# Optimization experiments

Measured on AMD Instinct MI355X. Metric: run time of the kernel, lower is better.

Reference implementation:

```python
import jax, jax.numpy as jnp
import numpy as np

H = 16          # num_heads
LN_EPS = 1e-5


def _layernorm(x, g, b):
    mu = jnp.mean(x, axis=-1, keepdims=True)
    var = jnp.mean(jnp.square(x - mu), axis=-1, keepdims=True)
    return (x - mu) * jax.lax.rsqrt(var + LN_EPS) * g + b


def setup_inputs() -> dict:
    key = jax.random.key(0)
    ks = jax.random.split(key, 4)
    B, T, D = 32, 1024, 1024
    s = 1.0 / np.sqrt(D)
    return {
        "x": jax.random.normal(ks[0], (B, T, D), dtype=jnp.float32),
        "ln_g": jnp.ones((D,), jnp.float32),
        "ln_b": jnp.zeros((D,), jnp.float32),
        "Wq": jax.random.normal(ks[1], (D, D), dtype=jnp.float32) * s,
        "bq": jnp.zeros((D,), jnp.float32),
        "Wk": jax.random.normal(ks[2], (D, D), dtype=jnp.float32) * s,
        "bk": jnp.zeros((D,), jnp.float32),
        "Wv": jax.random.normal(ks[3], (D, D), dtype=jnp.float32) * s,
        "bv": jnp.zeros((D,), jnp.float32),
    }


def reference(x, ln_g, ln_b, Wq, bq, Wk, bk, Wv, bv):
    B, T, D = x.shape
    d = D // H
    xn = _layernorm(x, ln_g, ln_b)                       # [B,T,D]
    # torch Linear: y = x @ W.T + b, W is [out, in]
    q = jnp.einsum('btd,ed->bte', xn, Wq) + bq
    k = jnp.einsum('btd,ed->bte', xn, Wk) + bk
    v = (jnp.einsum('btd,ed->bte', xn, Wv) + bv).reshape(B, T, H, d)
    q = jax.nn.softmax(q.reshape(B, T, H, d), axis=-1)   # softmax over head dim
    k = jax.nn.softmax(k.reshape(B, T, H, d), axis=1)    # softmax over sequence
    # linear attention: context [B,H,d,d], then project queries through it
    attn = jnp.einsum('bnhd,bnhl->bhdl', k, v)
    y = jnp.einsum('bnhd,bhdl->bnhl', q, attn).reshape(B, T, D)
    return x + y
```

## Files before the change

kernel.cpp:

```cpp
#include <hip/hip_runtime.h>
#include <stdint.h>

typedef __attribute__((ext_vector_type(4))) float  f32x4;
typedef __attribute__((ext_vector_type(8))) short  short8;
typedef __attribute__((ext_vector_type(2))) unsigned int uint2v;

#define DEV __device__ __forceinline__

DEV float b2f(unsigned short u) { return __uint_as_float(((unsigned)u) << 16); }
DEV unsigned short f2b(float f) {
  unsigned u = __float_as_uint(f);
  return (unsigned short)((u + 0x7fffu + ((u >> 16) & 1u)) >> 16);
}

#define AS1C(p) ((const __attribute__((address_space(1))) void*)(uintptr_t)(p))
#define AS3(p)  ((__attribute__((address_space(3))) void*)(unsigned)(uintptr_t)(p))
DEV void gload16(const void* g, void* l) {
  __builtin_amdgcn_global_load_lds(AS1C(g), AS3(l), 16, 0, 0);
}

static constexpr int B_ = 32, T_ = 1024, D_ = 1024;
static constexpr int M_ = B_ * T_;
static constexpr int N3 = 3 * D_;

__global__ __launch_bounds__(256) void cvt_weights(
    const float* __restrict__ Wq, const float* __restrict__ Wk, const float* __restrict__ Wv,
    const float* __restrict__ bq, const float* __restrict__ bk, const float* __restrict__ bv,
    unsigned short* __restrict__ Wcat, float* __restrict__ bias,
    float* __restrict__ ksum)
{
  int idx = blockIdx.x * 256 + threadIdx.x;
  int which = idx >> 18;
  int rem   = idx & 262143;
  const float* src = which == 0 ? Wq : (which == 1 ? Wk : Wv);
  f32x4 v = reinterpret_cast<const f32x4*>(src)[rem];
  uint2v p;
  p[0] = (unsigned)f2b(v[0]) | ((unsigned)f2b(v[1]) << 16);
  p[1] = (unsigned)f2b(v[2]) | ((unsigned)f2b(v[3]) << 16);
  reinterpret_cast<uint2v*>(Wcat)[idx] = p;
  if (idx < 3072) {
    const float* bsrc = idx < 1024 ? bq : (idx < 2048 ? bk : bv);
    bias[idx] = bsrc[idx & 1023];
  }
  if (idx < 32768) ksum[idx] = 0.f;
}

__global__ __launch_bounds__(256) void ln_kernel(
    const float* __restrict__ x, const float* __restrict__ g, const float* __restrict__ b,
    unsigned short* __restrict__ xn)
{
  int row = blockIdx.x;
  int tid = threadIdx.x;
  const f32x4 v = reinterpret_cast<const f32x4*>(x + (size_t)row * D_)[tid];
  float s  = v[0] + v[1] + v[2] + v[3];
  float s2 = v[0]*v[0] + v[1]*v[1] + v[2]*v[2] + v[3]*v[3];
  #pragma unroll
  for (int o = 32; o > 0; o >>= 1) { s += __shfl_down(s, o); s2 += __shfl_down(s2, o); }
  __shared__ float rs_[4], rs2_[4];
  int lane = tid & 63, wave = tid >> 6;
  if (lane == 0) { rs_[wave] = s; rs2_[wave] = s2; }
  __syncthreads();
  float S  = rs_[0] + rs_[1] + rs_[2] + rs_[3];
  float S2 = rs2_[0] + rs2_[1] + rs2_[2] + rs2_[3];
  float mu = S * (1.f / D_);
  float var = S2 * (1.f / D_) - mu * mu;
  float rstd = rsqrtf(var + 1e-5f);
  const f32x4 gg = reinterpret_cast<const f32x4*>(g)[tid];
  const f32x4 bb = reinterpret_cast<const f32x4*>(b)[tid];
  float y0 = (v[0]-mu)*rstd*gg[0] + bb[0];
  float y1 = (v[1]-mu)*rstd*gg[1] + bb[1];
  float y2 = (v[2]-mu)*rstd*gg[2] + bb[2];
  float y3 = (v[3]-mu)*rstd*gg[3] + bb[3];
  uint2v p;
  p[0] = (unsigned)f2b(y0) | ((unsigned)f2b(y1) << 16);
  p[1] = (unsigned)f2b(y2) | ((unsigned)f2b(y3) << 16);
  reinterpret_cast<uint2v*>(xn + (size_t)row * D_)[tid] = p;
}

__global__ __launch_bounds__(512, 2) void gemm_qkv(
    const unsigned short* __restrict__ A,
    const unsigned short* __restrict__ Bm,
    const float* __restrict__ bias,
    unsigned short* __restrict__ C,
    float* __restrict__ ksum)
{
  __shared__ alignas(16) short lds[4 * 16384];
  const int tid = threadIdx.x;
  constexpr int nbn = N3 / 256;
  constexpr int nwg = (M_ / 256) * nbn;
  int wg = blockIdx.x;
  int swzb = (wg & 7) * (nwg >> 3) + (wg >> 3);
  int bm = swzb / nbn, bn = swzb % nbn;
  int arow = bm * 256, bcol = bn * 256;
  int lane = tid & 63, wave = tid >> 6;
  int wr = wave >> 2, wc = wave & 3;
  int g = lane >> 4, r = lane & 15;

  const unsigned short* Ab = A  + (size_t)arow * 1024;
  const unsigned short* Bb = Bm + (size_t)bcol * 1024;

  int rho = (wave << 4) | (lane >> 2);
  int pg  = (lane & 3) ^ ((rho >> 1) & 3);
  size_t gR0 = (size_t)rho * 1024 + pg * 8;
  size_t gR1 = (size_t)(rho + 128) * 1024 + pg * 8;
  int lofs = wave * 512;

  #define STAGE_A(t) { short* bb0 = lds + (((t) & 3) << 14); int k2 = (t) << 5; \
    gload16(Ab + k2 + gR0, (void*)(bb0 + lofs)); \
    gload16(Ab + k2 + gR1, (void*)(bb0 + 4096 + lofs)); }
  #define STAGE_B(t) { short* bb0 = lds + (((t) & 3) << 14); int k2 = (t) << 5; \
    gload16(Bb + k2 + gR0, (void*)(bb0 + 8192 + lofs)); \
    gload16(Bb + k2 + gR1, (void*)(bb0 + 12288 + lofs)); }

  f32x4 acc[8][4] = {};
  STAGE_A(0); STAGE_B(0);
  STAGE_A(1); STAGE_B(1);
  STAGE_A(2); STAGE_B(2);
  asm volatile("s_waitcnt vmcnt(8)" ::: "memory");
  __builtin_amdgcn_s_barrier();

  for (int t = 0; t < 32; ++t) {
    const short* bufA = lds + ((t & 3) << 14);
    const short* bufB = bufA + 8192;
    short8 a0[4], b0[4];
    #pragma unroll
    for (int mi = 0; mi < 4; ++mi) {
      int row = wr * 128 + mi * 16 + r;
      a0[mi] = *(const short8*)(bufA + row * 32 + ((g ^ ((row >> 1) & 3)) << 3));
    }
    #pragma unroll
    for (int ni = 0; ni < 4; ++ni) {
      int row = wc * 64 + ni * 16 + r;
      b0[ni] = *(const short8*)(bufB + row * 32 + ((g ^ ((row >> 1) & 3)) << 3));
    }
    if (t < 29) STAGE_A(t + 3);
    __builtin_amdgcn_s_barrier();
    __builtin_amdgcn_s_setprio(1);
    #pragma unroll
    for (int mi = 0; mi < 4; ++mi)
      #pragma unroll
      for (int ni = 0; ni < 4; ++ni)
        acc[mi][ni] = __builtin_amdgcn_mfma_f32_16x16x32_bf16(a0[mi], b0[ni], acc[mi][ni], 0, 0, 0);
    __builtin_amdgcn_s_setprio(0);
    __builtin_amdgcn_s_barrier();
    short8 a1[4];
    #pragma unroll
    for (int mi = 0; mi < 4; ++mi) {
      int row = wr * 128 + (mi + 4) * 16 + r;
      a1[mi] = *(const short8*)(bufA + row * 32 + ((g ^ ((row >> 1) & 3)) << 3));
    }
    if (t < 29) STAGE_B(t + 3);
    __builtin_amdgcn_s_barrier();
    __builtin_amdgcn_s_setprio(1);
    #pragma unroll
    for (int mi = 0; mi < 4; ++mi)
      #pragma unroll
      for (int ni = 0; ni < 4; ++ni)
        acc[mi + 4][ni] = __builtin_amdgcn_mfma_f32_16x16x32_bf16(a1[mi], b0[ni], acc[mi + 4][ni], 0, 0, 0);
    __builtin_amdgcn_s_setprio(0);
    if (t < 29)       { asm volatile("s_waitcnt vmcnt(8)" ::: "memory"); }
    else if (t == 29) { asm volatile("s_waitcnt vmcnt(4)" ::: "memory"); }
    else if (t == 30) { asm volatile("s_waitcnt vmcnt(0)" ::: "memory"); }
    __builtin_amdgcn_s_barrier();
  }
  #undef STAGE_A
  #undef STAGE_B

  float bs[4];
  #pragma unroll
  for (int ni = 0; ni < 4; ++ni) bs[ni] = bias[bcol + wc * 64 + ni * 16 + r];
  bool isK = (bcol >= 1024 && bcol < 2048);
  if (isK) {
    float ks[4] = {0.f, 0.f, 0.f, 0.f};
    #pragma unroll
    for (int mi = 0; mi < 8; ++mi)
      #pragma unroll
      for (int j = 0; j < 4; ++j) {
        int rowl = wr * 128 + mi * 16 + 4 * g + j;
        size_t rb = (size_t)(arow + rowl) * N3 + bcol + wc * 64 + r;
        #pragma unroll
        for (int ni = 0; ni < 4; ++ni) {
          unsigned short cv = f2b(acc[mi][ni][j] + bs[ni]);
          C[rb + ni * 16] = cv;
          ks[ni] += __expf(b2f(cv));
        }
      }
    int b = arow >> 10;
    #pragma unroll
    for (int ni = 0; ni < 4; ++ni) {
      float s = ks[ni];
      s += __shfl_xor(s, 16);
      s += __shfl_xor(s, 32);
      if (g == 0)
        atomicAdd(&ksum[b * 1024 + (bcol - 1024) + wc * 64 + ni * 16 + r], s);
    }
  } else {
    #pragma unroll
    for (int mi = 0; mi < 8; ++mi)
      #pragma unroll
      for (int j = 0; j < 4; ++j) {
        int rowl = wr * 128 + mi * 16 + 4 * g + j;
        size_t rb = (size_t)(arow + rowl) * N3 + bcol + wc * 64 + r;
        #pragma unroll
        for (int ni = 0; ni < 4; ++ni)
          C[rb + ni * 16] = f2b(acc[mi][ni][j] + bs[ni]);
      }
  }
}

__global__ __launch_bounds__(256) void attn_kernel(
    const unsigned short* __restrict__ qkv, const float* __restrict__ ksum,
    unsigned short* __restrict__ attnT)
{
  int bh = blockIdx.x;
  int b = bh >> 4, h = bh & 15;
  int tid = threadIdx.x;
  int cgrp = tid & 7, trow = tid >> 3;
  int lane = tid & 63, wave = tid >> 6;
  int g = lane >> 4, r = lane & 15;
  __shared__ alignas(16) short lK[64 * 40];
  __shared__ alignas(16) short lV[64 * 40];
  const unsigned short* kb = qkv + (size_t)b * T_ * N3 + D_     + h * 64;
  const unsigned short* vb = qkv + (size_t)b * T_ * N3 + 2 * D_ + h * 64;
  float inv[8];
  const float* kp = ksum + b * 1024 + h * 64 + cgrp * 8;
  #pragma unroll
  for (int j = 0; j < 8; ++j) inv[j] = 1.f / kp[j];
  f32x4 acc[4] = {};
  for (int tc = 0; tc < 32; ++tc) {
    __syncthreads();
    int t0 = tc * 32;
    short8 kv = *(const short8*)(kb + (size_t)(t0 + trow) * N3 + cgrp * 8);
    short8 vv = *(const short8*)(vb + (size_t)(t0 + trow) * N3 + cgrp * 8);
    #pragma unroll
    for (int j = 0; j < 8; ++j) {
      lK[(cgrp * 8 + j) * 40 + trow] =
          (short)f2b(__expf(b2f((unsigned short)kv[j])) * inv[j]);
      lV[(cgrp * 8 + j) * 40 + trow] = vv[j];
    }
    __syncthreads();
    short8 af = *(const short8*)(lK + (16 * wave + r) * 40 + 8 * g);
    #pragma unroll
    for (int ni = 0; ni < 4; ++ni) {
      short8 bf = *(const short8*)(lV + (16 * ni + r) * 40 + 8 * g);
      acc[ni] = __builtin_amdgcn_mfma_f32_16x16x32_bf16(af, bf, acc[ni], 0, 0, 0);
    }
  }
  unsigned short* op = attnT + (size_t)bh * 4096;
  #pragma unroll
  for (int ni = 0; ni < 4; ++ni)
    #pragma unroll
    for (int j = 0; j < 4; ++j) {
      int m = 16 * wave + 4 * g + j;
      int n = 16 * ni + r;
      op[(size_t)n * 64 + m] = f2b(acc[ni][j]);
    }
}

__global__ __launch_bounds__(256) void out_kernel(
    const unsigned short* __restrict__ qkv, const unsigned short* __restrict__ attnT,
    const float* __restrict__ x, float* __restrict__ out)
{
  int bid = blockIdx.x;
  int bh = bid >> 3, mt = bid & 7;
  int b = bh >> 4, h = bh & 15;
  int tid = threadIdx.x;
  int lane = tid & 63, wave = tid >> 6;
  int g = lane >> 4, r = lane & 15;
  __shared__ alignas(16) short lAT[64 * 72];
  const unsigned short* at = attnT + (size_t)bh * 4096;
  #pragma unroll
  for (int i = 0; i < 2; ++i) {
    int idx8 = (i * 256 + tid) * 8;
    int n = idx8 >> 6, kk0 = idx8 & 63;
    *(short8*)(lAT + n * 72 + kk0) = *(const short8*)(at + idx8);
  }
  __syncthreads();
  short8 bt[4][2];
  #pragma unroll
  for (int ni = 0; ni < 4; ++ni)
    #pragma unroll
    for (int kc = 0; kc < 2; ++kc)
      bt[ni][kc] = *(const short8*)(lAT + (16 * ni + r) * 72 + kc * 32 + 8 * g);
  int rowbase = mt * 128 + 32 * wave;
  const unsigned short* qb = qkv + (size_t)(b * T_ + rowbase) * N3 + h * 64;
  short8 aq[2][2];
  #pragma unroll
  for (int mi = 0; mi < 2; ++mi) {
    float qe[16];
    float s = 0.f;
    #pragma unroll
    for (int kc = 0; kc < 2; ++kc) {
      short8 qa = *(const short8*)(qb + (size_t)(16 * mi + r) * N3 + kc * 32 + 8 * g);
      #pragma unroll
      for (int j = 0; j < 8; ++j) {
        float e = __expf(b2f((unsigned short)qa[j]));
        qe[kc * 8 + j] = e;
        s += e;
      }
    }
    s += __shfl_xor(s, 16);
    s += __shfl_xor(s, 32);
    float inv = 1.f / s;
    #pragma unroll
    for (int kc = 0; kc < 2; ++kc) {
      short8 t8;
      #pragma unroll
      for (int j = 0; j < 8; ++j) t8[j] = (short)f2b(qe[kc * 8 + j] * inv);
      aq[mi][kc] = t8;
    }
  }
  f32x4 acc[2][4] = {};
  #pragma unroll
  for (int mi = 0; mi < 2; ++mi)
    #pragma unroll
    for (int kc = 0; kc < 2; ++kc)
      #pragma unroll
      for (int ni = 0; ni < 4; ++ni)
        acc[mi][ni] = __builtin_amdgcn_mfma_f32_16x16x32_bf16(aq[mi][kc], bt[ni][kc], acc[mi][ni], 0, 0, 0);
  #pragma unroll
  for (int mi = 0; mi < 2; ++mi)
    #pragma unroll
    for (int ni = 0; ni < 4; ++ni)
      #pragma unroll
      for (int j = 0; j < 4; ++j) {
        int trow = rowbase + 16 * mi + 4 * g + j;
        int col  = h * 64 + 16 * ni + r;
        size_t gi = ((size_t)(b * T_ + trow) << 10) + col;
        out[gi] = x[gi] + acc[mi][ni][j];
      }
}

extern "C" void kernel_launch(void* const* d_in, const int* in_sizes, int n_in,
                              void* d_out, int out_size, void* d_ws, size_t ws_size,
                              hipStream_t stream) {
  const float* x   = (const float*)d_in[0];
  const float* lng = (const float*)d_in[1];
  const float* lnb = (const float*)d_in[2];
  const float* Wq  = (const float*)d_in[3];
  const float* bq  = (const float*)d_in[4];
  const float* Wk  = (const float*)d_in[5];
  const float* bk  = (const float*)d_in[6];
  const float* Wv  = (const float*)d_in[7];
  const float* bv  = (const float*)d_in[8];
  float* out = (float*)d_out;
  char* ws = (char*)d_ws;
  unsigned short* Wcat  = (unsigned short*)(ws + 0);
  float*          bias  = (float*)         (ws + 6291456);
  unsigned short* xn    = (unsigned short*)(ws + 6303744);
  unsigned short* qkv   = (unsigned short*)(ws + 73412608);
  unsigned short* attnT = (unsigned short*)(ws + 274739200);
  float* ksum = (float*)d_out;
  cvt_weights<<<3072,  256, 0, stream>>>(Wq, Wk, Wv, bq, bk, bv, Wcat, bias, ksum);
  ln_kernel  <<<M_,    256, 0, stream>>>(x, lng, lnb, xn);
  gemm_qkv   <<<1536,  512, 0, stream>>>(xn, Wcat, bias, qkv, ksum);
  attn_kernel<<<512,   256, 0, stream>>>(qkv, ksum, attnT);
  out_kernel <<<4096,  256, 0, stream>>>(qkv, attnT, x, out);
}
```

Baseline: 396.5 us.

## Split attention context over sequence chunks and coalesce output stores via LDS

The attention context kernel is split four ways along the sequence, giving 2048 blocks instead of 512. Each block writes fp32 partial sums into the reused xn buffer, and a new reduce kernel adds them and converts to bf16. The K/V global loads are also software-prefetched one chunk ahead. The output kernel stages its accumulators in LDS so the residual add and store become 16-byte coalesced vector accesses. The price is an extra kernel launch and partial-sum traffic, plus LDS use in the output kernel.

Result: faster. 379.6 us (-4.3%).

```diff
diff --git a/kernel.cpp b/kernel.cpp
--- a/kernel.cpp
+++ b/kernel.cpp
@@ -3,6 +3,7 @@
 
 typedef __attribute__((ext_vector_type(4))) float  f32x4;
 typedef __attribute__((ext_vector_type(8))) short  short8;
+typedef __attribute__((ext_vector_type(4))) short  short4v;
 typedef __attribute__((ext_vector_type(2))) unsigned int uint2v;
 
 #define DEV __device__ __forceinline__
@@ -210,9 +211,10 @@
 
 __global__ __launch_bounds__(256) void attn_kernel(
     const unsigned short* __restrict__ qkv, const float* __restrict__ ksum,
-    unsigned short* __restrict__ attnT)
-{
-  int bh = blockIdx.x;
+    float* __restrict__ attnP)
+{
+  int bid = blockIdx.x;
+  int bh = bid >> 2, tq = bid & 3;
   int b = bh >> 4, h = bh & 15;
   int tid = threadIdx.x;
   int cgrp = tid & 7, trow = tid >> 3;
@@ -220,18 +222,17 @@
   int g = lane >> 4, r = lane & 15;
   __shared__ alignas(16) short lK[64 * 40];
   __shared__ alignas(16) short lV[64 * 40];
-  const unsigned short* kb = qkv + (size_t)b * T_ * N3 + D_     + h * 64;
-  const unsigned short* vb = qkv + (size_t)b * T_ * N3 + 2 * D_ + h * 64;
+  const unsigned short* kb = qkv + ((size_t)(b * T_ + tq * 256)) * N3 + D_     + h * 64;
+  const unsigned short* vb = qkv + ((size_t)(b * T_ + tq * 256)) * N3 + 2 * D_ + h * 64;
   float inv[8];
   const float* kp = ksum + b * 1024 + h * 64 + cgrp * 8;
   #pragma unroll
   for (int j = 0; j < 8; ++j) inv[j] = 1.f / kp[j];
   f32x4 acc[4] = {};
-  for (int tc = 0; tc < 32; ++tc) {
+  short8 kv = *(const short8*)(kb + (size_t)trow * N3 + cgrp * 8);
+  short8 vv = *(const short8*)(vb + (size_t)trow * N3 + cgrp * 8);
+  for (int tc = 0; tc < 8; ++tc) {
     __syncthreads();
-    int t0 = tc * 32;
-    short8 kv = *(const short8*)(kb + (size_t)(t0 + trow) * N3 + cgrp * 8);
-    short8 vv = *(const short8*)(vb + (size_t)(t0 + trow) * N3 + cgrp * 8);
     #pragma unroll
     for (int j = 0; j < 8; ++j) {
       lK[(cgrp * 8 + j) * 40 + trow] =
@@ -239,6 +240,10 @@
       lV[(cgrp * 8 + j) * 40 + trow] = vv[j];
     }
     __syncthreads();
+    if (tc < 7) {
+      kv = *(const short8*)(kb + (size_t)((tc + 1) * 32 + trow) * N3 + cgrp * 8);
+      vv = *(const short8*)(vb + (size_t)((tc + 1) * 32 + trow) * N3 + cgrp * 8);
+    }
     short8 af = *(const short8*)(lK + (16 * wave + r) * 40 + 8 * g);
     #pragma unroll
     for (int ni = 0; ni < 4; ++ni) {
@@ -246,15 +251,40 @@
       acc[ni] = __builtin_amdgcn_mfma_f32_16x16x32_bf16(af, bf, acc[ni], 0, 0, 0);
     }
   }
-  unsigned short* op = attnT + (size_t)bh * 4096;
+  float* op = attnP + (size_t)bid * 4096;
   #pragma unroll
   for (int ni = 0; ni < 4; ++ni)
     #pragma unroll
     for (int j = 0; j < 4; ++j) {
       int m = 16 * wave + 4 * g + j;
       int n = 16 * ni + r;
-      op[(size_t)n * 64 + m] = f2b(acc[ni][j]);
-    }
+      op[(size_t)n * 64 + m] = acc[ni][j];
+    }
+}
+
+__global__ __launch_bounds__(256) void attn_reduce(
+    const float* __restrict__ attnP, unsigned short* __restrict__ attnT)
+{
+  int bh = blockIdx.x;
+  int tid = threadIdx.x;
+  const float* p0 = attnP + ((size_t)bh << 2) * 4096;
+  unsigned short* o = attnT + (size_t)bh * 4096;
+  #pragma unroll
+  for (int it = 0; it < 4; ++it) {
+    int i = (it * 256 + tid) * 4;
+    f32x4 s  = *(const f32x4*)(p0 + i);
+    f32x4 s1 = *(const f32x4*)(p0 + 4096 + i);
+    f32x4 s2 = *(const f32x4*)(p0 + 8192 + i);
+    f32x4 s3 = *(const f32x4*)(p0 + 12288 + i);
+    s[0] += s1[0] + s2[0] + s3[0];
+    s[1] += s1[1] + s2[1] + s3[1];
+    s[2] += s1[2] + s2[2] + s3[2];
+    s[3] += s1[3] + s2[3] + s3[3];
+    short4v ov;
+    ov[0] = (short)f2b(s[0]); ov[1] = (short)f2b(s[1]);
+    ov[2] = (short)f2b(s[2]); ov[3] = (short)f2b(s[3]);
+    *(short4v*)(o + i) = ov;
+  }
 }
 
 __global__ __launch_bounds__(256) void out_kernel(
@@ -268,6 +298,7 @@
   int lane = tid & 63, wave = tid >> 6;
   int g = lane >> 4, r = lane & 15;
   __shared__ alignas(16) short lAT[64 * 72];
+  __shared__ float lO[128][66];
   const unsigned short* at = attnT + (size_t)bh * 4096;
   #pragma unroll
   for (int i = 0; i < 2; ++i) {
@@ -323,12 +354,22 @@
     #pragma unroll
     for (int ni = 0; ni < 4; ++ni)
       #pragma unroll
-      for (int j = 0; j < 4; ++j) {
-        int trow = rowbase + 16 * mi + 4 * g + j;
-        int col  = h * 64 + 16 * ni + r;
-        size_t gi = ((size_t)(b * T_ + trow) << 10) + col;
-        out[gi] = x[gi] + acc[mi][ni][j];
-      }
+      for (int j = 0; j < 4; ++j)
+        lO[32 * wave + 16 * mi + 4 * g + j][16 * ni + r] = acc[mi][ni][j];
+  __syncthreads();
+  int rr = tid >> 4, c4 = (tid & 15) << 2;
+  #pragma unroll
+  for (int p = 0; p < 8; ++p) {
+    int rowl = p * 16 + rr;
+    size_t gi = ((size_t)(b * T_ + mt * 128 + rowl) << 10) + h * 64 + c4;
+    f32x4 xv = *(const f32x4*)(x + gi);
+    f32x4 ov;
+    ov[0] = xv[0] + lO[rowl][c4];
+    ov[1] = xv[1] + lO[rowl][c4 + 1];
+    ov[2] = xv[2] + lO[rowl][c4 + 2];
+    ov[3] = xv[3] + lO[rowl][c4 + 3];
+    *(f32x4*)(out + gi) = ov;
+  }
 }
 
 extern "C" void kernel_launch(void* const* d_in, const int* in_sizes, int n_in,
@@ -350,10 +391,12 @@
   unsigned short* xn    = (unsigned short*)(ws + 6303744);
   unsigned short* qkv   = (unsigned short*)(ws + 73412608);
   unsigned short* attnT = (unsigned short*)(ws + 274739200);
+  float* attnP = (float*)xn;
   float* ksum = (float*)d_out;
   cvt_weights<<<3072,  256, 0, stream>>>(Wq, Wk, Wv, bq, bk, bv, Wcat, bias, ksum);
   ln_kernel  <<<M_,    256, 0, stream>>>(x, lng, lnb, xn);
   gemm_qkv   <<<1536,  512, 0, stream>>>(xn, Wcat, bias, qkv, ksum);
-  attn_kernel<<<512,   256, 0, stream>>>(qkv, ksum, attnT);
+  attn_kernel<<<2048,  256, 0, stream>>>(qkv, ksum, attnP);
+  attn_reduce<<<512,   256, 0, stream>>>(attnP, attnT);
   out_kernel <<<4096,  256, 0, stream>>>(qkv, attnT, x, out);
 }
```
